# Kernel tuning notes

Hardware: AMD Instinct MI355X
Metric: run time of the kernel (lower is better)

## Reference

```python
import jax, jax.numpy as jnp
import numpy as np

DIM = 1024
NUM_HEADS = 16
BATCH = 4
SEQ = 2048
SCALE = (DIM // NUM_HEADS) ** -0.5
MASK_VAL = -10000000.0


def setup_inputs() -> dict:
    key = jax.random.key(0)
    k1, k2, k3, k4 = jax.random.split(key, 4)
    inputs = jax.random.normal(k1, (BATCH, SEQ, DIM), dtype=jnp.float32)
    # xavier-ish scaling for weights
    W_qkv = jax.random.normal(k2, (3 * DIM, DIM), dtype=jnp.float32) * (1.0 / np.sqrt(DIM))
    W_fc = jax.random.normal(k3, (DIM, DIM), dtype=jnp.float32) * (1.0 / np.sqrt(DIM))
    b_fc = jnp.zeros((DIM,), dtype=jnp.float32)
    padding_mask = jax.random.randint(k4, (BATCH, SEQ), 0, 2, dtype=jnp.int32)
    return {"inputs": inputs, "W_qkv": W_qkv, "W_fc": W_fc, "b_fc": b_fc,
            "padding_mask": padding_mask}


def reference(inputs, W_qkv, W_fc, b_fc, padding_mask):
    B, N, C = inputs.shape
    H = NUM_HEADS
    Dh = C // H
    # qkv projection (torch Linear: x @ W.T), [B,N,3C]
    qkv = jnp.einsum('bnc,oc->bno', inputs, W_qkv)
    qkv = qkv.reshape(B, N, 3, H, Dh).transpose(2, 0, 3, 1, 4)  # [3,B,H,N,Dh]
    q, k, v = qkv[0], qkv[1], qkv[2]
    att = jnp.einsum('bhqd,bhkd->bhqk', q, k) * SCALE  # [B,H,N,N]
    mask = padding_mask[:, None, None, :]              # [B,1,1,N]
    att = jnp.where(mask > 0, jnp.float32(MASK_VAL), att)
    att = jax.nn.softmax(att, axis=-1)
    x = jnp.einsum('bhqk,bhkd->bhqd', att, v)          # [B,H,N,Dh]
    x = x.transpose(0, 2, 1, 3).reshape(B, N, C)       # [B,N,C]
    out = jnp.einsum('bnc,oc->bno', x, W_fc) + b_fc
    return out
```

## Files before the change

kernel.cpp:

```cpp
#include <hip/hip_runtime.h>
#include <stdint.h>

constexpr int kDim  = 1024;
constexpr int kH    = 16;
constexpr int kB    = 4;
constexpr int kSeq  = 2048;
constexpr int kDh   = 64;
constexpr int kMTot = kB * kSeq;
constexpr int kNQkv = 3 * kDim;
constexpr float kScale = 0.125f;
constexpr float kLog2e = 1.44269504088896f;
constexpr float kC1    = kScale * kLog2e;
constexpr float kMaxSub = 10.0f;
constexpr float kMk2Un   = -kMaxSub * kLog2e;
constexpr float kMk2Mask = -1.0e9f;
constexpr int kPld = 72;
constexpr int kCld = 136;

typedef __attribute__((ext_vector_type(8))) short short8;
typedef __attribute__((ext_vector_type(4))) float floatx4;

__device__ __forceinline__ unsigned short f2bf(float f) {
  union { float f; unsigned u; } v; v.f = f;
  unsigned r = v.u + 0x7fffu + ((v.u >> 16) & 1u);
  return (unsigned short)(r >> 16);
}
__device__ __forceinline__ unsigned short f2bf_fast(float f) {
  union { float f; unsigned u; } v; v.f = f;
  return (unsigned short)((v.u + 0x8000u) >> 16);
}
__device__ __forceinline__ float vexp2(float x) {
  float r; asm("v_exp_f32 %0, %1" : "=v"(r) : "v"(x)); return r;
}
__device__ __forceinline__ void gl2lds16(const void* g, void* l) {
  __builtin_amdgcn_global_load_lds(
      (const __attribute__((address_space(1))) unsigned int*)g,
      (__attribute__((address_space(3))) unsigned int*)l, 16, 0, 0);
}

__global__ void __launch_bounds__(256) cvt_scan(
    const float4* __restrict__ x, const float4* __restrict__ wq,
    const float4* __restrict__ wf,
    ushort4* __restrict__ xb, ushort4* __restrict__ wqb, ushort4* __restrict__ wfb,
    const int* __restrict__ pm, int* __restrict__ cidx, int* __restrict__ nkd,
    int* __restrict__ ctr) {
  const int X4  = (kMTot * kDim) / 4;
  const int WQ4 = (kNQkv * kDim) / 4;
  const int NCVT = 12288;
  if (blockIdx.x >= NCVT) {
    const int b = blockIdx.x - NCVT;
    const int t = threadIdx.x;
    const int lane = t & 63, wv = t >> 6;
    __shared__ int wsum[4];
    __shared__ int woff[5];
    if (b == 0 && t == 0) *ctr = 256;
    int base = t * 8;
    int keep[8]; int cnt = 0;
#pragma unroll
    for (int j = 0; j < 8; j++) {
      keep[j] = (pm[b * kSeq + base + j] <= 0) ? 1 : 0;
      cnt += keep[j];
    }
    int pre = cnt;
#pragma unroll
    for (int off = 1; off < 64; off <<= 1) {
      int v = __shfl_up(pre, off, 64);
      if (lane >= off) pre += v;
    }
    int excl = pre - cnt;
    if (lane == 63) wsum[wv] = pre;
    __syncthreads();
    if (t == 0) {
      int s = 0;
#pragma unroll
      for (int w = 0; w < 4; w++) { woff[w] = s; s += wsum[w]; }
      woff[4] = s;
      nkd[b] = s;
    }
    __syncthreads();
    const int nk = woff[4];
    int kp = woff[wv] + excl;
#pragma unroll
    for (int j = 0; j < 8; j++) {
      int n = base + j;
      int pos = keep[j] ? kp : nk + (n - kp);
      cidx[b * kSeq + pos] = b * kSeq + n;
      kp += keep[j];
    }
    return;
  }
  int i = blockIdx.x * 256 + threadIdx.x;
  float4 v; ushort4* dst;
  if (i < X4)            { v = x[i];             dst = xb  + i; }
  else if (i < X4 + WQ4) { v = wq[i - X4];       dst = wqb + (i - X4); }
  else                   { v = wf[i - X4 - WQ4]; dst = wfb + (i - X4 - WQ4); }
  ushort4 o;
  o.x = f2bf(v.x); o.y = f2bf(v.y); o.z = f2bf(v.z); o.w = f2bf(v.w);
  *dst = o;
}

__global__ void __launch_bounds__(512, 2) gemm_qkv(
    const unsigned short* __restrict__ xb, const unsigned short* __restrict__ wqb,
    const int* __restrict__ cidx, const int* __restrict__ nkd,
    int* __restrict__ ctr,
    unsigned short* __restrict__ qb, unsigned short* __restrict__ kb,
    unsigned short* __restrict__ vtb) {
  extern __shared__ __attribute__((aligned(16))) unsigned short smem[];
  __shared__ int s_slot;
  unsigned short* As0 = smem;
  unsigned short* Bs0 = smem + 16384;
  unsigned short* As1 = smem + 32768;
  unsigned short* Bs1 = smem + 49152;

  const int t = threadIdx.x;
  const int lane = t & 63, wv = t >> 6;
  const int wm = (wv >> 2) << 7;
  const int wn = (wv & 3) << 6;
  const int lrow = lane & 15, quad = lane >> 4, l7 = lane & 7;
  const int srow = t >> 3;
  const int pu8 = (t & 7) * 8;
  const int lu8 = ((t & 7) ^ (srow & 7)) * 8;
  const int off0 = (quad ^ l7) * 8;

  const int rr0 = (nkd[0] + 127) >> 7, rr1 = (nkd[1] + 127) >> 7;
  const int rr2 = (nkd[2] + 127) >> 7, rr3 = (nkd[3] + 127) >> 7;
  const int tb0 = (rr0 + 1) >> 1, tb1 = (rr1 + 1) >> 1;
  const int tb2 = (rr2 + 1) >> 1, tb3 = (rr3 + 1) >> 1;
  const int pA = tb0, pB = pA + tb1, pC = pB + tb2, pD = pC + tb3;
  const int NT = 128 + 8 * pD;

#define STAGE_B(buf, p, k0) gl2lds16(brow + (int64_t)(p) * 64 * kDim + (k0), \
                                     (buf) + ((p) * 64 + srow) * 64 + pu8)
#define STAGE_A(buf, p, k0) gl2lds16(arow[p] + (k0), \
                                     (buf) + ((p) * 64 + srow) * 64 + pu8)
#define BARRIER() { asm volatile("" ::: "memory"); \
                    __builtin_amdgcn_s_barrier(); \
                    asm volatile("" ::: "memory"); }

  int slot = blockIdx.x;
  while (slot < NT) {
    int which, tN, tMl, bb, rbv;
    if (slot < 128) {
      which = 0; tN = (slot & 3) * 256;
      int tMg = (slot >> 2) * 256;
      bb = tMg >> 11; tMl = tMg & 2047; rbv = 16;
    } else {
      int id = slot - 128;
      const int TK = 4 * pD;
      which = (id < TK) ? 1 : 2;
      if (which == 2) id -= TK;
      int col = id & 3, j = id >> 2;
      int pj;
      if (j < pA)      { bb = 0; pj = j;      rbv = rr0; }
      else if (j < pB) { bb = 1; pj = j - pA; rbv = rr1; }
      else if (j < pC) { bb = 2; pj = j - pB; rbv = rr2; }
      else             { bb = 3; pj = j - pC; rbv = rr3; }
      tMl = pj * 256;
      tN = (which == 1 ? 1024 : 2048) + col * 256;
    }
    int nrows;
    if (which == 0) nrows = 256;
    else { int rem = rbv * 128 - tMl; nrows = (rem >= 256) ? 256 : 128; }
    const bool na4 = (nrows == 256);
    const bool act = (wm < nrows);
    const bool vblk = (which == 2);

    const unsigned short* arow[4];
#pragma unroll
    for (int p = 0; p < 4; p++) {
      int pe = (!na4 && p > 1) ? 1 : p;
      int rl = tMl + pe * 64 + srow;
      int rid = (which == 0) ? (bb * 2048 + rl) : cidx[bb * 2048 + rl];
      arow[p] = xb + (int64_t)rid * kDim + lu8;
    }
    const unsigned short* brow = wqb + (int64_t)(tN + srow) * kDim + lu8;

    floatx4 acc[8][4];
    floatx4 zero = {0.f, 0.f, 0.f, 0.f};
#pragma unroll
    for (int mi = 0; mi < 8; mi++)
#pragma unroll
      for (int ni = 0; ni < 4; ni++) acc[mi][ni] = zero;

    STAGE_B(Bs0, 0, 0); STAGE_B(Bs0, 1, 0); STAGE_B(Bs0, 2, 0); STAGE_B(Bs0, 3, 0);
    STAGE_A(As0, 0, 0); STAGE_A(As0, 1, 0);
    if (na4) { STAGE_A(As0, 2, 0); STAGE_A(As0, 3, 0); }
    STAGE_B(Bs1, 0, 64); STAGE_B(Bs1, 1, 64); STAGE_B(Bs1, 2, 64); STAGE_B(Bs1, 3, 64);
    STAGE_A(As1, 0, 64); STAGE_A(As1, 1, 64);
    if (na4) { STAGE_A(As1, 2, 64); STAGE_A(As1, 3, 64); }
    if (na4) { asm volatile("s_waitcnt vmcnt(8)" ::: "memory"); }
    else     { asm volatile("s_waitcnt vmcnt(6)" ::: "memory"); }
    BARRIER();

    for (int tt = 0; tt < 16; ++tt) {
      const unsigned short* Ac = (tt & 1) ? As1 : As0;
      const unsigned short* Bc = (tt & 1) ? Bs1 : Bs0;
      unsigned short* An = (tt & 1) ? As0 : As1;
      unsigned short* Bn = (tt & 1) ? Bs0 : Bs1;

      if (tt >= 1 && tt < 15) {
        const int kn = (tt + 1) * 64;
        STAGE_B(Bn, 0, kn); STAGE_B(Bn, 1, kn); STAGE_B(Bn, 2, kn); STAGE_B(Bn, 3, kn);
        STAGE_A(An, 0, kn); STAGE_A(An, 1, kn);
        if (na4) { STAGE_A(An, 2, kn); STAGE_A(An, 3, kn); }
      }

      if (act) {
#pragma unroll
        for (int kk = 0; kk < 64; kk += 32) {
          short8 bf[4], af[8];
#pragma unroll
          for (int ni = 0; ni < 4; ni++)
            bf[ni] = *(const short8*)(Bc + (wn + ni * 16 + lrow) * 64 + (off0 ^ kk));
#pragma unroll
          for (int mi = 0; mi < 8; mi++)
            af[mi] = *(const short8*)(Ac + (wm + mi * 16 + lrow) * 64 + (off0 ^ kk));
#pragma unroll
          for (int mi = 0; mi < 8; mi++)
#pragma unroll
            for (int ni = 0; ni < 4; ni++)
              acc[mi][ni] = __builtin_amdgcn_mfma_f32_16x16x32_bf16(af[mi], bf[ni], acc[mi][ni], 0, 0, 0);
        }
      }

      asm volatile("s_waitcnt vmcnt(0)" ::: "memory");
      BARRIER();
    }

    unsigned short* Cs = smem;
    const int h4 = (tN >> 6) & 15;
#pragma unroll
    for (int h = 0; h < 2; h++) {
      const bool writer = ((((wv & 3) >> 1) == h) && act);
      const int cwn = (wv & 1) * 64;
      if (!vblk) {
        if (writer) {
#pragma unroll
          for (int mi = 0; mi < 8; mi++)
#pragma unroll
            for (int ni = 0; ni < 4; ni++)
#pragma unroll
              for (int r = 0; r < 4; r++) {
                int row = wm + mi * 16 + quad * 4 + r;
                int c = cwn + ni * 16 + lrow;
                Cs[row * kCld + c] = f2bf(acc[mi][ni][r]);
              }
        }
        asm volatile("s_waitcnt lgkmcnt(0)" ::: "memory");
        BARRIER();
        unsigned short* qk = (which == 0) ? qb : kb;
        const int itn = nrows >> 6;
#pragma unroll
        for (int g = 0; g < 2; g++) {
          int hh = (h4 + h * 2 + g) & 15;
          unsigned short* base = qk + ((int64_t)((bb << 4) + hh) << 17)
                                 + (int64_t)tMl * 64;
          for (int it = 0; it < itn; it++) {
            int off = it * 4096 + t * 8;
            int n = off >> 6;
            int d = off & 63;
            *(short8*)(base + off) = *(const short8*)(Cs + n * kCld + g * 64 + d);
          }
        }
        BARRIER();
      } else {
        if (writer) {
#pragma unroll
          for (int mi = 0; mi < 8; mi++)
#pragma unroll
            for (int ni = 0; ni < 4; ni++)
#pragma unroll
              for (int r = 0; r < 4; r++) {
                int row = wm + mi * 16 + quad * 4 + r;
                int c = cwn + ni * 16 + lrow;
                Cs[c * 264 + row] = f2bf(acc[mi][ni][r]);
              }
        }
        asm volatile("s_waitcnt lgkmcnt(0)" ::: "memory");
        BARRIER();
        const int c8n = nrows >> 3;
#pragma unroll
        for (int g = 0; g < 2; g++) {
          int hh = (h4 + h * 2 + g) & 15;
          unsigned short* vbase = vtb + (((int64_t)((bb << 4) + hh)) << 17) + tMl;
#pragma unroll
          for (int it = 0; it < 4; it++) {
            int off = it * 512 + t;
            int d = off >> 5, c8 = off & 31;
            if (c8 < c8n)
              *(short8*)(vbase + (int64_t)d * 2048 + c8 * 8) =
                  *(const short8*)(Cs + (g * 64 + d) * 264 + c8 * 8);
          }
        }
        BARRIER();
      }
    }

    if (t == 0) s_slot = atomicAdd(ctr, 1);
    __syncthreads();
    slot = s_slot;
  }
#undef STAGE_B
#undef STAGE_A
#undef BARRIER
}

__global__ void __launch_bounds__(256, 4) attn(
    const unsigned short* __restrict__ qb, const unsigned short* __restrict__ kb,
    const unsigned short* __restrict__ vtb, const int* __restrict__ nkd,
    unsigned short* __restrict__ xab) {
  __shared__ __attribute__((aligned(16))) unsigned short Ks[64 * 64];
  __shared__ __attribute__((aligned(16))) unsigned short Vs[64 * 64];
  __shared__ __attribute__((aligned(16))) unsigned short Ps[4][2][16 * kPld];

  const int t = threadIdx.x, lane = t & 63, wv = t >> 6;
  const int lrow = lane & 15, quad = lane >> 4, l7 = lane & 7;
  const int qblk = blockIdx.x & 15, bh = blockIdx.x >> 4;
  const int b = bh >> 4, h = bh & 15;
  const int q0 = qblk * 128;
  const int srow = t >> 3;
  const int pu8 = (t & 7) * 8;
  const int lu8 = ((t & 7) ^ (srow & 7)) * 8;
  const int off0 = (quad ^ l7) * 8;

  const int nk  = nkd[b];
  const int nkt = (nk + 63) >> 6;

  const unsigned short* Qb0 = qb + ((int64_t)bh * kSeq + q0 + wv * 16 + lrow) * kDh;
  short8 qf[2][2];
  qf[0][0] = *(const short8*)(Qb0 + quad * 8);
  qf[0][1] = *(const short8*)(Qb0 + 32 + quad * 8);
  qf[1][0] = *(const short8*)(Qb0 + 64 * kDh + quad * 8);
  qf[1][1] = *(const short8*)(Qb0 + 64 * kDh + 32 + quad * 8);

  float l_run[2][4];
  floatx4 o_acc[2][4];
  floatx4 zero = {0.f, 0.f, 0.f, 0.f};
#pragma unroll
  for (int t2 = 0; t2 < 2; t2++) {
#pragma unroll
    for (int r = 0; r < 4; r++) l_run[t2][r] = 0.f;
#pragma unroll
    for (int di = 0; di < 4; di++) o_acc[t2][di] = zero;
  }

  const unsigned short* Kbase = kb  + (int64_t)bh * kSeq * kDh;
  const unsigned short* Vbase = vtb + (int64_t)bh * kDh * kSeq;

  for (int kt = 0; kt < nkt; ++kt) {
    const int k0 = kt * 64;
    {
      int r0 = srow, r1 = srow + 32;
      gl2lds16(Kbase + (int64_t)(k0 + r0) * kDh + lu8, Ks + r0 * 64 + pu8);
      gl2lds16(Kbase + (int64_t)(k0 + r1) * kDh + lu8, Ks + r1 * 64 + pu8);
      gl2lds16(Vbase + (int64_t)r0 * kSeq + k0 + lu8,  Vs + r0 * 64 + pu8);
      gl2lds16(Vbase + (int64_t)r1 * kSeq + k0 + lu8,  Vs + r1 * 64 + pu8);
    }
    __syncthreads();

    floatx4 s[2][4];
#pragma unroll
    for (int ni = 0; ni < 4; ni++) {
      const unsigned short* Kr = Ks + (ni * 16 + lrow) * 64;
      short8 kf0 = *(const short8*)(Kr + off0);
      short8 kf1 = *(const short8*)(Kr + (off0 ^ 32));
#pragma unroll
      for (int t2 = 0; t2 < 2; t2++) {
        floatx4 tmp = __builtin_amdgcn_mfma_f32_16x16x32_bf16(qf[t2][0], kf0, zero, 0, 0, 0);
        s[t2][ni]   = __builtin_amdgcn_mfma_f32_16x16x32_bf16(qf[t2][1], kf1, tmp, 0, 0, 0);
      }
    }
    float mk2[4];
#pragma unroll
    for (int c = 0; c < 4; c++)
      mk2[c] = (k0 + c * 16 + lrow < nk) ? kMk2Un : kMk2Mask;

#pragma unroll
    for (int t2 = 0; t2 < 2; t2++) {
      unsigned short* Pw = &Ps[wv][t2][0];
#pragma unroll
      for (int r = 0; r < 4; r++) {
        int prow = (quad * 4 + r) * kPld + lrow;
#pragma unroll
        for (int c = 0; c < 4; c++) {
          float p = vexp2(fmaf(s[t2][c][r], kC1, mk2[c]));
          l_run[t2][r] += p;
          Pw[prow + c * 16] = f2bf_fast(p);
        }
      }
    }
    asm volatile("s_waitcnt lgkmcnt(0)" ::: "memory");

#pragma unroll
    for (int ks = 0; ks < 2; ks++) {
      short8 pf0 = *(const short8*)(&Ps[wv][0][0] + lrow * kPld + ks * 32 + quad * 8);
      short8 pf1 = *(const short8*)(&Ps[wv][1][0] + lrow * kPld + ks * 32 + quad * 8);
      const int voff = off0 ^ (ks * 32);
#pragma unroll
      for (int di = 0; di < 4; di++) {
        short8 vf = *(const short8*)(Vs + (di * 16 + lrow) * 64 + voff);
        o_acc[0][di] = __builtin_amdgcn_mfma_f32_16x16x32_bf16(pf0, vf, o_acc[0][di], 0, 0, 0);
        o_acc[1][di] = __builtin_amdgcn_mfma_f32_16x16x32_bf16(pf1, vf, o_acc[1][di], 0, 0, 0);
      }
    }
    __syncthreads();
  }

#pragma unroll
  for (int t2 = 0; t2 < 2; t2++) {
#pragma unroll
    for (int r = 0; r < 4; r++) {
      float l = l_run[t2][r];
      l += __shfl_xor(l, 1, 64);
      l += __shfl_xor(l, 2, 64);
      l += __shfl_xor(l, 4, 64);
      l += __shfl_xor(l, 8, 64);
      float inv = 1.0f / l;
      int n = q0 + t2 * 64 + wv * 16 + quad * 4 + r;
      int64_t rowbase = ((int64_t)b * kSeq + n) * kDim + h * kDh;
#pragma unroll
      for (int di = 0; di < 4; di++)
        xab[rowbase + di * 16 + lrow] = f2bf(o_acc[t2][di][r] * inv);
    }
  }
}

__global__ void __launch_bounds__(256) gemm_fc(
    const unsigned short* __restrict__ xab, const unsigned short* __restrict__ wfb,
    const float* __restrict__ bfc, float* __restrict__ out) {
  __shared__ __attribute__((aligned(16))) unsigned short As[128 * 64];
  __shared__ __attribute__((aligned(16))) unsigned short Bs[128 * 64];
  const int tN = blockIdx.x * 128, tM = blockIdx.y * 128;
  const int t = threadIdx.x;
  const int lane = t & 63, wv = t >> 6;
  const int wm = (wv >> 1) << 6, wn = (wv & 1) << 6;
  const int lrow = lane & 15, quad = lane >> 4, l7 = lane & 7;
  const int srow = t >> 3;
  const int pu8 = (t & 7) * 8;
  const int lu8 = ((t & 7) ^ (srow & 7)) * 8;
  const int off0 = (quad ^ l7) * 8;

  floatx4 acc[4][4];
  floatx4 zero = {0.f, 0.f, 0.f, 0.f};
#pragma unroll
  for (int mi = 0; mi < 4; mi++)
#pragma unroll
    for (int ni = 0; ni < 4; ni++) acc[mi][ni] = zero;

  for (int k0 = 0; k0 < kDim; k0 += 64) {
#pragma unroll
    for (int p = 0; p < 4; ++p) {
      int r = srow + p * 32;
      gl2lds16(xab + (int64_t)(tM + r) * kDim + k0 + lu8, As + r * 64 + pu8);
      gl2lds16(wfb + (int64_t)(tN + r) * kDim + k0 + lu8, Bs + r * 64 + pu8);
    }
    __syncthreads();
#pragma unroll
    for (int kk = 0; kk < 64; kk += 32) {
      short8 af[4], bf[4];
#pragma unroll
      for (int mi = 0; mi < 4; mi++)
        af[mi] = *(const short8*)(As + (wm + mi * 16 + lrow) * 64 + (off0 ^ kk));
#pragma unroll
      for (int ni = 0; ni < 4; ni++)
        bf[ni] = *(const short8*)(Bs + (wn + ni * 16 + lrow) * 64 + (off0 ^ kk));
#pragma unroll
      for (int mi = 0; mi < 4; mi++)
#pragma unroll
        for (int ni = 0; ni < 4; ni++)
          acc[mi][ni] = __builtin_amdgcn_mfma_f32_16x16x32_bf16(af[mi], bf[ni], acc[mi][ni], 0, 0, 0);
    }
    __syncthreads();
  }

#pragma unroll
  for (int ni = 0; ni < 4; ni++) {
    int o = tN + wn + ni * 16 + lrow;
    float bias = bfc[o];
#pragma unroll
    for (int mi = 0; mi < 4; mi++) {
#pragma unroll
      for (int r = 0; r < 4; r++) {
        int i = tM + wm + mi * 16 + quad * 4 + r;
        out[(int64_t)i * kDim + o] = acc[mi][ni][r] + bias;
      }
    }
  }
}

extern "C" void kernel_launch(void* const* d_in, const int* in_sizes, int n_in,
                              void* d_out, int out_size, void* d_ws, size_t ws_size,
                              hipStream_t stream) {
  (void)in_sizes; (void)n_in; (void)out_size; (void)ws_size;
  const float* x    = (const float*)d_in[0];
  const float* wqkv = (const float*)d_in[1];
  const float* wfc  = (const float*)d_in[2];
  const float* bfc  = (const float*)d_in[3];
  const int*   pm   = (const int*)d_in[4];
  float* out = (float*)d_out;

  char* ws = (char*)d_ws;
  unsigned short* xb  = (unsigned short*)(ws);
  unsigned short* wqb = (unsigned short*)(ws + 16777216);
  unsigned short* wfb = (unsigned short*)(ws + 23068672);
  unsigned short* qb  = (unsigned short*)(ws + 25165824);
  unsigned short* kb  = (unsigned short*)(ws + 41943040);
  unsigned short* vtb = (unsigned short*)(ws + 58720256);
  int*            cidx= (int*)(ws + 75497472);
  int*            nkd = (int*)(ws + 75530240);
  int*            ctr = (int*)(ws + 75530256);
  unsigned short* xab = xb;

  static bool s_attr_set = false;
  if (!s_attr_set) {
    (void)hipFuncSetAttribute((const void*)gemm_qkv,
                              hipFuncAttributeMaxDynamicSharedMemorySize, 131072);
    s_attr_set = true;
  }

  cvt_scan<<<12288 + kB, 256, 0, stream>>>(
      (const float4*)x, (const float4*)wqkv, (const float4*)wfc,
      (ushort4*)xb, (ushort4*)wqb, (ushort4*)wfb, pm, cidx, nkd, ctr);
  gemm_qkv<<<256, 512, 131072, stream>>>(
      xb, wqb, cidx, nkd, ctr, qb, kb, vtb);
  attn<<<kB * kH * (kSeq / 128), 256, 0, stream>>>(qb, kb, vtb, nkd, xab);
  gemm_fc<<<dim3(kDim / 128, kMTot / 128), 256, 0, stream>>>(xab, wfb, bfc, out);
}
```

Before: 228.8 us.

## Use 4-stage K=32 LDS ring pipeline in QKV and FC GEMMs

The QKV GEMM's double-buffered K=64 staging becomes a four-slot ring of K=32 half-tiles. Loads run two steps ahead, and a partial vmcnt wait replaces the full drain before each barrier. The FC GEMM is rewritten the same way: 512 threads, 256x128 tiles and 96KB of dynamic LDS, replacing the old single-buffered 128x128 kernel that synchronized twice per step. The aim is to hide global-to-LDS latency and reduce stalls, at the cost of more barriers per K and a new swizzle that must stay correct.

Result: slower. 236.0 us (+3.1%).

```diff
diff --git a/kernel.cpp b/kernel.cpp
--- a/kernel.cpp
+++ b/kernel.cpp
@@ -107,20 +107,17 @@
     unsigned short* __restrict__ vtb) {
   extern __shared__ __attribute__((aligned(16))) unsigned short smem[];
   __shared__ int s_slot;
-  unsigned short* As0 = smem;
-  unsigned short* Bs0 = smem + 16384;
-  unsigned short* As1 = smem + 32768;
-  unsigned short* Bs1 = smem + 49152;
 
   const int t = threadIdx.x;
   const int lane = t & 63, wv = t >> 6;
   const int wm = (wv >> 2) << 7;
   const int wn = (wv & 3) << 6;
-  const int lrow = lane & 15, quad = lane >> 4, l7 = lane & 7;
-  const int srow = t >> 3;
-  const int pu8 = (t & 7) * 8;
-  const int lu8 = ((t & 7) ^ (srow & 7)) * 8;
-  const int off0 = (quad ^ l7) * 8;
+  const int lrow = lane & 15, quad = lane >> 4;
+  const int offh = ((quad ^ ((lrow & 3) ^ ((lrow >> 2) & 3))) << 3);
+  const int rQ   = t >> 2;
+  const int sT   = ((t >> 2) & 3) ^ ((t >> 4) & 3);
+  const int lc8  = (((t & 3) ^ sT) << 3);
+  const int tOff = t * 8;
 
   const int rr0 = (nkd[0] + 127) >> 7, rr1 = (nkd[1] + 127) >> 7;
   const int rr2 = (nkd[2] + 127) >> 7, rr3 = (nkd[3] + 127) >> 7;
@@ -129,13 +126,15 @@
   const int pA = tb0, pB = pA + tb1, pC = pB + tb2, pD = pC + tb3;
   const int NT = 128 + 8 * pD;
 
-#define STAGE_B(buf, p, k0) gl2lds16(brow + (int64_t)(p) * 64 * kDim + (k0), \
-                                     (buf) + ((p) * 64 + srow) * 64 + pu8)
-#define STAGE_A(buf, p, k0) gl2lds16(arow[p] + (k0), \
-                                     (buf) + ((p) * 64 + srow) * 64 + pu8)
 #define BARRIER() { asm volatile("" ::: "memory"); \
                     __builtin_amdgcn_s_barrier(); \
                     asm volatile("" ::: "memory"); }
+#define STAGEH(h) { unsigned short* Hb_ = smem + ((h) & 3) * 16384; \
+    const int ko_ = (h) * 32; \
+    gl2lds16(aS0 + ko_, Hb_ + tOff); \
+    if (na4) gl2lds16(aS1 + ko_, Hb_ + 4096 + tOff); \
+    gl2lds16(bS0 + ko_, Hb_ + 8192 + tOff); \
+    gl2lds16(bS1 + ko_, Hb_ + 12288 + tOff); }
 
   int slot = blockIdx.x;
   while (slot < NT) {
@@ -165,15 +164,15 @@
     const bool act = (wm < nrows);
     const bool vblk = (which == 2);
 
-    const unsigned short* arow[4];
-#pragma unroll
-    for (int p = 0; p < 4; p++) {
-      int pe = (!na4 && p > 1) ? 1 : p;
-      int rl = tMl + pe * 64 + srow;
-      int rid = (which == 0) ? (bb * 2048 + rl) : cidx[bb * 2048 + rl];
-      arow[p] = xb + (int64_t)rid * kDim + lu8;
-    }
-    const unsigned short* brow = wqb + (int64_t)(tN + srow) * kDim + lu8;
+    const int gBase = bb * 2048 + tMl;
+    int g0 = gBase + rQ;
+    int g1 = gBase + (na4 ? 128 + rQ : rQ);
+    int r0 = (which == 0) ? g0 : cidx[g0];
+    int r1 = (which == 0) ? g1 : cidx[g1];
+    const unsigned short* aS0 = xb + (int64_t)r0 * kDim + lc8;
+    const unsigned short* aS1 = xb + (int64_t)r1 * kDim + lc8;
+    const unsigned short* bS0 = wqb + (int64_t)(tN + rQ) * kDim + lc8;
+    const unsigned short* bS1 = wqb + (int64_t)(tN + 128 + rQ) * kDim + lc8;
 
     floatx4 acc[8][4];
     floatx4 zero = {0.f, 0.f, 0.f, 0.f};
@@ -182,48 +181,36 @@
 #pragma unroll
       for (int ni = 0; ni < 4; ni++) acc[mi][ni] = zero;
 
-    STAGE_B(Bs0, 0, 0); STAGE_B(Bs0, 1, 0); STAGE_B(Bs0, 2, 0); STAGE_B(Bs0, 3, 0);
-    STAGE_A(As0, 0, 0); STAGE_A(As0, 1, 0);
-    if (na4) { STAGE_A(As0, 2, 0); STAGE_A(As0, 3, 0); }
-    STAGE_B(Bs1, 0, 64); STAGE_B(Bs1, 1, 64); STAGE_B(Bs1, 2, 64); STAGE_B(Bs1, 3, 64);
-    STAGE_A(As1, 0, 64); STAGE_A(As1, 1, 64);
-    if (na4) { STAGE_A(As1, 2, 64); STAGE_A(As1, 3, 64); }
-    if (na4) { asm volatile("s_waitcnt vmcnt(8)" ::: "memory"); }
-    else     { asm volatile("s_waitcnt vmcnt(6)" ::: "memory"); }
+    STAGEH(0); STAGEH(1);
+    if (na4) { asm volatile("s_waitcnt vmcnt(4)" ::: "memory"); }
+    else     { asm volatile("s_waitcnt vmcnt(3)" ::: "memory"); }
     BARRIER();
 
-    for (int tt = 0; tt < 16; ++tt) {
-      const unsigned short* Ac = (tt & 1) ? As1 : As0;
-      const unsigned short* Bc = (tt & 1) ? Bs1 : Bs0;
-      unsigned short* An = (tt & 1) ? As0 : As1;
-      unsigned short* Bn = (tt & 1) ? Bs0 : Bs1;
-
-      if (tt >= 1 && tt < 15) {
-        const int kn = (tt + 1) * 64;
-        STAGE_B(Bn, 0, kn); STAGE_B(Bn, 1, kn); STAGE_B(Bn, 2, kn); STAGE_B(Bn, 3, kn);
-        STAGE_A(An, 0, kn); STAGE_A(An, 1, kn);
-        if (na4) { STAGE_A(An, 2, kn); STAGE_A(An, 3, kn); }
-      }
-
+#pragma unroll 4
+    for (int hs = 0; hs < 32; ++hs) {
+      if (hs < 30) STAGEH(hs + 2);
       if (act) {
-#pragma unroll
-        for (int kk = 0; kk < 64; kk += 32) {
-          short8 bf[4], af[8];
+        const unsigned short* HA = smem + (hs & 3) * 16384;
+        const unsigned short* HB = HA + 8192;
+        short8 bf[4], af[8];
+#pragma unroll
+        for (int ni = 0; ni < 4; ni++)
+          bf[ni] = *(const short8*)(HB + (wn + ni * 16 + lrow) * 32 + offh);
+#pragma unroll
+        for (int mi = 0; mi < 8; mi++)
+          af[mi] = *(const short8*)(HA + (wm + mi * 16 + lrow) * 32 + offh);
+#pragma unroll
+        for (int mi = 0; mi < 8; mi++)
 #pragma unroll
           for (int ni = 0; ni < 4; ni++)
-            bf[ni] = *(const short8*)(Bc + (wn + ni * 16 + lrow) * 64 + (off0 ^ kk));
-#pragma unroll
-          for (int mi = 0; mi < 8; mi++)
-            af[mi] = *(const short8*)(Ac + (wm + mi * 16 + lrow) * 64 + (off0 ^ kk));
-#pragma unroll
-          for (int mi = 0; mi < 8; mi++)
-#pragma unroll
-            for (int ni = 0; ni < 4; ni++)
-              acc[mi][ni] = __builtin_amdgcn_mfma_f32_16x16x32_bf16(af[mi], bf[ni], acc[mi][ni], 0, 0, 0);
-        }
-      }
-
-      asm volatile("s_waitcnt vmcnt(0)" ::: "memory");
+            acc[mi][ni] = __builtin_amdgcn_mfma_f32_16x16x32_bf16(af[mi], bf[ni], acc[mi][ni], 0, 0, 0);
+      }
+      if (hs < 30) {
+        if (na4) { asm volatile("s_waitcnt vmcnt(4)" ::: "memory"); }
+        else     { asm volatile("s_waitcnt vmcnt(3)" ::: "memory"); }
+      } else {
+        asm volatile("s_waitcnt vmcnt(0)" ::: "memory");
+      }
       BARRIER();
     }
 
@@ -300,8 +287,7 @@
     __syncthreads();
     slot = s_slot;
   }
-#undef STAGE_B
-#undef STAGE_A
+#undef STAGEH
 #undef BARRIER
 }
 
@@ -425,60 +411,78 @@
   }
 }
 
-__global__ void __launch_bounds__(256) gemm_fc(
+__global__ void __launch_bounds__(512, 2) gemm_fc(
     const unsigned short* __restrict__ xab, const unsigned short* __restrict__ wfb,
     const float* __restrict__ bfc, float* __restrict__ out) {
-  __shared__ __attribute__((aligned(16))) unsigned short As[128 * 64];
-  __shared__ __attribute__((aligned(16))) unsigned short Bs[128 * 64];
-  const int tN = blockIdx.x * 128, tM = blockIdx.y * 128;
+  extern __shared__ __attribute__((aligned(16))) unsigned short smem[];
   const int t = threadIdx.x;
   const int lane = t & 63, wv = t >> 6;
-  const int wm = (wv >> 1) << 6, wn = (wv & 1) << 6;
-  const int lrow = lane & 15, quad = lane >> 4, l7 = lane & 7;
-  const int srow = t >> 3;
-  const int pu8 = (t & 7) * 8;
-  const int lu8 = ((t & 7) ^ (srow & 7)) * 8;
-  const int off0 = (quad ^ l7) * 8;
-
-  floatx4 acc[4][4];
+  const int wm = (wv >> 2) << 7;
+  const int wn = (wv & 3) << 5;
+  const int lrow = lane & 15, quad = lane >> 4;
+  const int offh = ((quad ^ ((lrow & 3) ^ ((lrow >> 2) & 3))) << 3);
+  const int rQ   = t >> 2;
+  const int sT   = ((t >> 2) & 3) ^ ((t >> 4) & 3);
+  const int lc8  = (((t & 3) ^ sT) << 3);
+  const int tOff = t * 8;
+  const int tN = blockIdx.x * 128, tM = blockIdx.y * 256;
+
+  const unsigned short* aS0 = xab + (int64_t)(tM + rQ) * kDim + lc8;
+  const unsigned short* aS1 = xab + (int64_t)(tM + 128 + rQ) * kDim + lc8;
+  const unsigned short* bS0 = wfb + (int64_t)(tN + rQ) * kDim + lc8;
+
+#define BARRIER() { asm volatile("" ::: "memory"); \
+                    __builtin_amdgcn_s_barrier(); \
+                    asm volatile("" ::: "memory"); }
+#define STAGEF(h) { unsigned short* Hb_ = smem + ((h) & 3) * 12288; \
+    const int ko_ = (h) * 32; \
+    gl2lds16(aS0 + ko_, Hb_ + tOff); \
+    gl2lds16(aS1 + ko_, Hb_ + 4096 + tOff); \
+    gl2lds16(bS0 + ko_, Hb_ + 8192 + tOff); }
+
+  floatx4 acc[8][2];
   floatx4 zero = {0.f, 0.f, 0.f, 0.f};
 #pragma unroll
-  for (int mi = 0; mi < 4; mi++)
-#pragma unroll
-    for (int ni = 0; ni < 4; ni++) acc[mi][ni] = zero;
-
-  for (int k0 = 0; k0 < kDim; k0 += 64) {
-#pragma unroll
-    for (int p = 0; p < 4; ++p) {
-      int r = srow + p * 32;
-      gl2lds16(xab + (int64_t)(tM + r) * kDim + k0 + lu8, As + r * 64 + pu8);
-      gl2lds16(wfb + (int64_t)(tN + r) * kDim + k0 + lu8, Bs + r * 64 + pu8);
-    }
-    __syncthreads();
-#pragma unroll
-    for (int kk = 0; kk < 64; kk += 32) {
-      short8 af[4], bf[4];
-#pragma unroll
-      for (int mi = 0; mi < 4; mi++)
-        af[mi] = *(const short8*)(As + (wm + mi * 16 + lrow) * 64 + (off0 ^ kk));
-#pragma unroll
-      for (int ni = 0; ni < 4; ni++)
-        bf[ni] = *(const short8*)(Bs + (wn + ni * 16 + lrow) * 64 + (off0 ^ kk));
-#pragma unroll
-      for (int mi = 0; mi < 4; mi++)
-#pragma unroll
-        for (int ni = 0; ni < 4; ni++)
+  for (int mi = 0; mi < 8; mi++)
+#pragma unroll
+    for (int ni = 0; ni < 2; ni++) acc[mi][ni] = zero;
+
+  STAGEF(0); STAGEF(1);
+  asm volatile("s_waitcnt vmcnt(3)" ::: "memory");
+  BARRIER();
+
+#pragma unroll 4
+  for (int hs = 0; hs < 32; ++hs) {
+    if (hs < 30) STAGEF(hs + 2);
+    {
+      const unsigned short* HA = smem + (hs & 3) * 12288;
+      const unsigned short* HB = HA + 8192;
+      short8 bf[2], af[8];
+#pragma unroll
+      for (int ni = 0; ni < 2; ni++)
+        bf[ni] = *(const short8*)(HB + (wn + ni * 16 + lrow) * 32 + offh);
+#pragma unroll
+      for (int mi = 0; mi < 8; mi++)
+        af[mi] = *(const short8*)(HA + (wm + mi * 16 + lrow) * 32 + offh);
+#pragma unroll
+      for (int mi = 0; mi < 8; mi++)
+#pragma unroll
+        for (int ni = 0; ni < 2; ni++)
           acc[mi][ni] = __builtin_amdgcn_mfma_f32_16x16x32_bf16(af[mi], bf[ni], acc[mi][ni], 0, 0, 0);
     }
-    __syncthreads();
-  }
-
-#pragma unroll
-  for (int ni = 0; ni < 4; ni++) {
+    if (hs < 30) { asm volatile("s_waitcnt vmcnt(3)" ::: "memory"); }
+    else         { asm volatile("s_waitcnt vmcnt(0)" ::: "memory"); }
+    BARRIER();
+  }
+#undef STAGEF
+#undef BARRIER
+
+#pragma unroll
+  for (int ni = 0; ni < 2; ni++) {
     int o = tN + wn + ni * 16 + lrow;
     float bias = bfc[o];
 #pragma unroll
-    for (int mi = 0; mi < 4; mi++) {
+    for (int mi = 0; mi < 8; mi++) {
 #pragma unroll
       for (int r = 0; r < 4; r++) {
         int i = tM + wm + mi * 16 + quad * 4 + r;
@@ -515,6 +519,8 @@
   if (!s_attr_set) {
     (void)hipFuncSetAttribute((const void*)gemm_qkv,
                               hipFuncAttributeMaxDynamicSharedMemorySize, 131072);
+    (void)hipFuncSetAttribute((const void*)gemm_fc,
+                              hipFuncAttributeMaxDynamicSharedMemorySize, 98304);
     s_attr_set = true;
   }
 
@@ -524,5 +530,5 @@
   gemm_qkv<<<256, 512, 131072, stream>>>(
       xb, wqb, cidx, nkd, ctr, qb, kb, vtb);
   attn<<<kB * kH * (kSeq / 128), 256, 0, stream>>>(qb, kb, vtb, nkd, xab);
-  gemm_fc<<<dim3(kDim / 128, kMTot / 128), 256, 0, stream>>>(xab, wfb, bfc, out);
-}
+  gemm_fc<<<dim3(kDim / 128, kMTot / 256), 512, 98304, stream>>>(xab, wfb, bfc, out);
+}
```
